# Optimization experiments

Measured on AMD Instinct MI355X. Metric: run time of the kernel, lower is better.

The kernel has to match this reference:

```python
import jax, jax.numpy as jnp
import numpy as np

QMAX = 127.0  # torch.iinfo(torch.int8).max


def setup_inputs() -> dict:
    key = jax.random.key(0)
    k1, k2 = jax.random.split(key)
    input_act = jax.random.normal(k1, (4, 2048, 4096), dtype=jnp.float32)
    # nn.Linear weight: [out_features, in_features], fp weights pre-quantization
    weight = jax.random.normal(k2, (4096, 4096), dtype=jnp.float32) * 0.02
    return {"input_act": input_act, "weight": weight}


def reference(input_act, weight):
    # --- weight_quant (per-channel over in_features) ---
    w_scale = jnp.max(jnp.abs(weight), axis=-1, keepdims=True) / QMAX      # [O, 1]
    w_q = jnp.round(weight / w_scale).astype(jnp.int8)                      # int8 weight

    # --- activation quant (per-token over last dim) ---
    a_scale = jnp.max(jnp.abs(input_act), axis=-1, keepdims=True) / QMAX    # [B, S, 1]
    x_q = jnp.round(input_act / a_scale).astype(jnp.int8)                   # int8 acts

    # --- int8 GEMM with int32 accumulation (torch._int_mm semantics) ---
    # [B, S, K] @ [K, O] -> [B, S, O]
    acc = jnp.matmul(x_q.astype(jnp.int32), w_q.T.astype(jnp.int32))        # exact int32

    # --- dequant: scale = input_act_scale * weight_scale.T, then cast to fp16 ---
    scale = a_scale * w_scale.T[None, :, :]                                 # [B, S, O]
    out = (acc.astype(jnp.float32) * scale).astype(jnp.float16)
    return out
```

## Files before the change

### kernel.cpp

```cpp
#include <hip/hip_runtime.h>
#include <hip/hip_fp16.h>
#include <cstdint>

typedef int v4i __attribute__((ext_vector_type(4)));

#define AS1C(p) ((const __attribute__((address_space(1))) void*)(p))
#define AS3(p)  ((__attribute__((address_space(3))) void*)(p))

__global__ __launch_bounds__(256) void quant_rows(const float* __restrict__ X,
                                                  int8_t* __restrict__ Q,
                                                  float* __restrict__ scales,
                                                  int K) {
    const int row = blockIdx.x;
    const float4* xv = (const float4*)(X + (size_t)row * K);

    float4 v[4];
#pragma unroll
    for (int j = 0; j < 4; ++j) v[j] = xv[threadIdx.x + (j << 8)];

    float m = 0.0f;
#pragma unroll
    for (int j = 0; j < 4; ++j) {
        m = fmaxf(m, fmaxf(fmaxf(fabsf(v[j].x), fabsf(v[j].y)),
                           fmaxf(fabsf(v[j].z), fabsf(v[j].w))));
    }
    for (int off = 32; off > 0; off >>= 1)
        m = fmaxf(m, __shfl_xor(m, off, 64));

    __shared__ float wmax[4];
    __shared__ float s_sc;
    const int lane = threadIdx.x & 63;
    const int wv = threadIdx.x >> 6;
    if (lane == 0) wmax[wv] = m;
    __syncthreads();
    if (threadIdx.x == 0) {
        float mm = fmaxf(fmaxf(wmax[0], wmax[1]), fmaxf(wmax[2], wmax[3]));
        float sc = mm / 127.0f;
        scales[row] = sc;
        s_sc = sc;
    }
    __syncthreads();
    const float sc = s_sc;

    char4* qv = (char4*)(Q + (size_t)row * K);
#pragma unroll
    for (int j = 0; j < 4; ++j) {
        char4 q;
        q.x = (signed char)(int)rintf(v[j].x / sc);
        q.y = (signed char)(int)rintf(v[j].y / sc);
        q.z = (signed char)(int)rintf(v[j].z / sc);
        q.w = (signed char)(int)rintf(v[j].w / sc);
        qv[threadIdx.x + (j << 8)] = q;
    }
}

__global__ __launch_bounds__(512, 2) void gemm_i8(const int8_t* __restrict__ Aq,
                                                  const int8_t* __restrict__ Bq,
                                                  const float* __restrict__ a_scale,
                                                  const float* __restrict__ w_scale,
                                                  float* __restrict__ out) {
    extern __shared__ __align__(16) int8_t smem[];

    const int K = 4096;
    const int bid = blockIdx.x;
    const int wg  = (bid & 7) * 64 + (bid >> 3);
    const int n0 = (wg & 15) * 256;
    const int m0 = (wg >> 4) * 256;

    const int tid  = threadIdx.x;
    const int lane = tid & 63;
    const int wid  = tid >> 6;
    const int wm   = wid >> 2;
    const int wn   = wid & 3;

    const int rsel  = lane & 15;
    const int kswz  = ((lane >> 4) << 4) ^ (((rsel >> 1) & 3) << 4);
    const int abase = (wm * 128 + rsel) * 64 + kswz;
    const int bbase = 16384 + (wn * 64 + rsel) * 64 + kswz;

    const int strow = tid >> 2;
    const int stswz = ((strow >> 1) & 3) << 4;
    const int stcol = ((tid & 3) << 4) ^ stswz;
    const int8_t* gA = Aq + (size_t)(m0 + strow) * K + stcol;
    const int8_t* gB = Bq + (size_t)(n0 + strow) * K + stcol;
    const size_t rstep = (size_t)128 * K;
    const int ldsst = wid * 1024;

    v4i acc[8][4] = {};
    v4i aFa[8], aFb[8], bFa[4], bFb[4];

#define STAGE(buf, kt) do {                                                          \
    int8_t* _d = smem + (buf) * 32768;                                               \
    const int8_t* _a = gA + (size_t)(kt) * 64;                                       \
    const int8_t* _b = gB + (size_t)(kt) * 64;                                       \
    __builtin_amdgcn_global_load_lds(AS1C(_a),         AS3(_d + ldsst),         16, 0, 0); \
    __builtin_amdgcn_global_load_lds(AS1C(_a + rstep), AS3(_d + 8192  + ldsst), 16, 0, 0); \
    __builtin_amdgcn_global_load_lds(AS1C(_b),         AS3(_d + 16384 + ldsst), 16, 0, 0); \
    __builtin_amdgcn_global_load_lds(AS1C(_b + rstep), AS3(_d + 24576 + ldsst), 16, 0, 0); \
  } while (0)

#define GROUP(g, CA, CB, NA, NB, gsrc, goff)  do {                                   \
    NA[2*(g)]     = *(const v4i*)(bufN + abase + (2*(g))     * 1024);                \
    NA[2*(g) + 1] = *(const v4i*)(bufN + abase + (2*(g) + 1) * 1024);                \
    NB[(g)]       = *(const v4i*)(bufN + bbase + (g) * 1024);                        \
    __builtin_amdgcn_global_load_lds(AS1C(gsrc), AS3(pD + (goff) + ldsst), 16, 0, 0);\
    _Pragma("unroll")                                                                \
    for (int nt = 0; nt < 4; ++nt) {                                                 \
        acc[2*(g)][nt] = __builtin_amdgcn_mfma_i32_16x16x64_i8(                      \
            CA[2*(g)], CB[nt], acc[2*(g)][nt], 0, 0, 0);                             \
        acc[2*(g)+1][nt] = __builtin_amdgcn_mfma_i32_16x16x64_i8(                    \
            CA[2*(g)+1], CB[nt], acc[2*(g)+1][nt], 0, 0, 0);                         \
    }                                                                                \
  } while (0)

#define KSTEP(u, CA, CB, NA, NB, kt4) do {                                           \
    const int kt  = (kt4) + (u);                                                     \
    const int8_t* bufN = smem + (((u) + 1) & 3) * 32768;                             \
    int8_t* pD = smem + (((u) + 3) & 3) * 32768;                                     \
    const int ktp = (kt + 3 < 64) ? (kt + 3) : 63;                                   \
    const int8_t* _a = gA + (size_t)ktp * 64;                                        \
    const int8_t* _b = gB + (size_t)ktp * 64;                                        \
    asm volatile("s_waitcnt vmcnt(4)" ::: "memory");                                 \
    __builtin_amdgcn_s_barrier();                                                    \
    __builtin_amdgcn_s_setprio(1);                                                   \
    GROUP(0, CA, CB, NA, NB, _a,         0);                                         \
    __builtin_amdgcn_sched_barrier(0);                                               \
    GROUP(1, CA, CB, NA, NB, _a + rstep, 8192);                                      \
    __builtin_amdgcn_sched_barrier(0);                                               \
    GROUP(2, CA, CB, NA, NB, _b,         16384);                                     \
    __builtin_amdgcn_sched_barrier(0);                                               \
    GROUP(3, CA, CB, NA, NB, _b + rstep, 24576);                                     \
    __builtin_amdgcn_s_setprio(0);                                                   \
  } while (0)

    STAGE(0, 0); STAGE(1, 1); STAGE(2, 2);
    asm volatile("s_waitcnt vmcnt(8)" ::: "memory");
    __builtin_amdgcn_s_barrier();
#pragma unroll
    for (int mt = 0; mt < 8; ++mt) aFa[mt] = *(const v4i*)(smem + abase + mt * 1024);
#pragma unroll
    for (int nt = 0; nt < 4; ++nt) bFa[nt] = *(const v4i*)(smem + bbase + nt * 1024);

    for (int kt4 = 0; kt4 < 64; kt4 += 4) {
        KSTEP(0, aFa, bFa, aFb, bFb, kt4);
        KSTEP(1, aFb, bFb, aFa, bFa, kt4);
        KSTEP(2, aFa, bFa, aFb, bFb, kt4);
        KSTEP(3, aFb, bFb, aFa, bFa, kt4);
    }

    const int r0  = (lane >> 4) << 2;
    const int col = lane & 15;
#pragma unroll
    for (int mt = 0; mt < 8; ++mt) {
        const int tbase = m0 + wm * 128 + mt * 16 + r0;
        float as[4];
#pragma unroll
        for (int r = 0; r < 4; ++r) as[r] = a_scale[tbase + r];
#pragma unroll
        for (int nt = 0; nt < 4; ++nt) {
            const int o = n0 + wn * 64 + nt * 16 + col;
            const float wsc = w_scale[o];
#pragma unroll
            for (int r = 0; r < 4; ++r) {
                float v = (float)acc[mt][nt][r] * as[r] * wsc;
                out[(size_t)(tbase + r) * 4096 + o] = __half2float(__float2half_rn(v));
            }
        }
    }
#undef KSTEP
#undef GROUP
#undef STAGE
}

extern "C" void kernel_launch(void* const* d_in, const int* in_sizes, int n_in,
                              void* d_out, int out_size, void* d_ws, size_t ws_size,
                              hipStream_t stream) {
    const float* input_act = (const float*)d_in[0];
    const float* weight    = (const float*)d_in[1];
    float* out = (float*)d_out;

    const int K = 4096, O = 4096, T = 8192;

    int8_t* x_q = (int8_t*)d_ws;
    int8_t* w_q = x_q + (size_t)T * K;
    float* a_scale = (float*)(w_q + (size_t)O * K);
    float* w_scale = a_scale + T;

    static bool attr_done = false;
    if (!attr_done) {
        hipFuncSetAttribute(reinterpret_cast<const void*>(gemm_i8),
                            hipFuncAttributeMaxDynamicSharedMemorySize, 131072);
        attr_done = true;
    }

    quant_rows<<<T, 256, 0, stream>>>(input_act, x_q, a_scale, K);
    quant_rows<<<O, 256, 0, stream>>>(weight, w_q, w_scale, K);

    dim3 grid(512);
    gemm_i8<<<grid, 512, 131072, stream>>>(x_q, w_q, a_scale, w_scale, out);
}
```

Before: 180.8 us.

## Fuse quant kernels and stagger MFMA/LDS-read phases across wave halves

Merges the activation and weight quantization launches into one kernel with a combined grid, removing one launch and the tail gap between them. In the GEMM main loop, the first four waves issue their LDS reads before the MFMAs in each group, while the other four waves issue MFMAs first and then reads. The setprio raise now wraps only the MFMA blocks. The intent is a ping-pong schedule in which one half of the waves keeps the matrix units busy while the other half loads fragments, at the cost of duplicated loop code and a changed register schedule.

```diff
diff --git a/kernel.cpp b/kernel.cpp
--- a/kernel.cpp
+++ b/kernel.cpp
@@ -7,12 +7,23 @@
 #define AS1C(p) ((const __attribute__((address_space(1))) void*)(p))
 #define AS3(p)  ((__attribute__((address_space(3))) void*)(p))
 
-__global__ __launch_bounds__(256) void quant_rows(const float* __restrict__ X,
-                                                  int8_t* __restrict__ Q,
-                                                  float* __restrict__ scales,
-                                                  int K) {
+__global__ __launch_bounds__(256) void quant_fused(const float* __restrict__ X,
+                                                   const float* __restrict__ W,
+                                                   int8_t* __restrict__ Xq,
+                                                   int8_t* __restrict__ Wq,
+                                                   float* __restrict__ a_scale,
+                                                   float* __restrict__ w_scale) {
     const int row = blockIdx.x;
-    const float4* xv = (const float4*)(X + (size_t)row * K);
+    const float* src;
+    int8_t* dst;
+    float* scp;
+    if (row < 8192) {
+        src = X + (size_t)row * 4096;  dst = Xq + (size_t)row * 4096;  scp = a_scale + row;
+    } else {
+        const int r = row - 8192;
+        src = W + (size_t)r * 4096;    dst = Wq + (size_t)r * 4096;    scp = w_scale + r;
+    }
+    const float4* xv = (const float4*)src;
 
     float4 v[4];
 #pragma unroll
@@ -36,13 +47,13 @@
     if (threadIdx.x == 0) {
         float mm = fmaxf(fmaxf(wmax[0], wmax[1]), fmaxf(wmax[2], wmax[3]));
         float sc = mm / 127.0f;
-        scales[row] = sc;
+        *scp = sc;
         s_sc = sc;
     }
     __syncthreads();
     const float sc = s_sc;
 
-    char4* qv = (char4*)(Q + (size_t)row * K);
+    char4* qv = (char4*)dst;
 #pragma unroll
     for (int j = 0; j < 4; ++j) {
         char4 q;
@@ -99,11 +110,15 @@
     __builtin_amdgcn_global_load_lds(AS1C(_b + rstep), AS3(_d + 24576 + ldsst), 16, 0, 0); \
   } while (0)
 
-#define GROUP(g, CA, CB, NA, NB, gsrc, goff)  do {                                   \
+#define READS(g, NA, NB, gsrc, goff) do {                                            \
     NA[2*(g)]     = *(const v4i*)(bufN + abase + (2*(g))     * 1024);                \
     NA[2*(g) + 1] = *(const v4i*)(bufN + abase + (2*(g) + 1) * 1024);                \
     NB[(g)]       = *(const v4i*)(bufN + bbase + (g) * 1024);                        \
     __builtin_amdgcn_global_load_lds(AS1C(gsrc), AS3(pD + (goff) + ldsst), 16, 0, 0);\
+  } while (0)
+
+#define MFMAS(g, CA, CB) do {                                                        \
+    __builtin_amdgcn_s_setprio(1);                                                   \
     _Pragma("unroll")                                                                \
     for (int nt = 0; nt < 4; ++nt) {                                                 \
         acc[2*(g)][nt] = __builtin_amdgcn_mfma_i32_16x16x64_i8(                      \
@@ -111,9 +126,24 @@
         acc[2*(g)+1][nt] = __builtin_amdgcn_mfma_i32_16x16x64_i8(                    \
             CA[2*(g)+1], CB[nt], acc[2*(g)+1][nt], 0, 0, 0);                         \
     }                                                                                \
-  } while (0)
-
-#define KSTEP(u, CA, CB, NA, NB, kt4) do {                                           \
+    __builtin_amdgcn_s_setprio(0);                                                   \
+  } while (0)
+
+#define GROUP_RW(g, CA, CB, NA, NB, gsrc, goff)  do {                                \
+    READS(g, NA, NB, gsrc, goff);                                                    \
+    __builtin_amdgcn_sched_barrier(0);                                               \
+    MFMAS(g, CA, CB);                                                                \
+    __builtin_amdgcn_sched_barrier(0);                                               \
+  } while (0)
+
+#define GROUP_WR(g, CA, CB, NA, NB, gsrc, goff)  do {                                \
+    MFMAS(g, CA, CB);                                                                \
+    __builtin_amdgcn_sched_barrier(0);                                               \
+    READS(g, NA, NB, gsrc, goff);                                                    \
+    __builtin_amdgcn_sched_barrier(0);                                               \
+  } while (0)
+
+#define KSTEP(G, u, CA, CB, NA, NB, kt4) do {                                        \
     const int kt  = (kt4) + (u);                                                     \
     const int8_t* bufN = smem + (((u) + 1) & 3) * 32768;                             \
     int8_t* pD = smem + (((u) + 3) & 3) * 32768;                                     \
@@ -122,15 +152,11 @@
     const int8_t* _b = gB + (size_t)ktp * 64;                                        \
     asm volatile("s_waitcnt vmcnt(4)" ::: "memory");                                 \
     __builtin_amdgcn_s_barrier();                                                    \
-    __builtin_amdgcn_s_setprio(1);                                                   \
-    GROUP(0, CA, CB, NA, NB, _a,         0);                                         \
-    __builtin_amdgcn_sched_barrier(0);                                               \
-    GROUP(1, CA, CB, NA, NB, _a + rstep, 8192);                                      \
-    __builtin_amdgcn_sched_barrier(0);                                               \
-    GROUP(2, CA, CB, NA, NB, _b,         16384);                                     \
-    __builtin_amdgcn_sched_barrier(0);                                               \
-    GROUP(3, CA, CB, NA, NB, _b + rstep, 24576);                                     \
-    __builtin_amdgcn_s_setprio(0);                                                   \
+    __builtin_amdgcn_sched_barrier(0);                                               \
+    G(0, CA, CB, NA, NB, _a,         0);                                             \
+    G(1, CA, CB, NA, NB, _a + rstep, 8192);                                          \
+    G(2, CA, CB, NA, NB, _b,         16384);                                         \
+    G(3, CA, CB, NA, NB, _b + rstep, 24576);                                         \
   } while (0)
 
     STAGE(0, 0); STAGE(1, 1); STAGE(2, 2);
@@ -141,11 +167,20 @@
 #pragma unroll
     for (int nt = 0; nt < 4; ++nt) bFa[nt] = *(const v4i*)(smem + bbase + nt * 1024);
 
-    for (int kt4 = 0; kt4 < 64; kt4 += 4) {
-        KSTEP(0, aFa, bFa, aFb, bFb, kt4);
-        KSTEP(1, aFb, bFb, aFa, bFa, kt4);
-        KSTEP(2, aFa, bFa, aFb, bFb, kt4);
-        KSTEP(3, aFb, bFb, aFa, bFa, kt4);
+    if (wid < 4) {
+        for (int kt4 = 0; kt4 < 64; kt4 += 4) {
+            KSTEP(GROUP_RW, 0, aFa, bFa, aFb, bFb, kt4);
+            KSTEP(GROUP_RW, 1, aFb, bFb, aFa, bFa, kt4);
+            KSTEP(GROUP_RW, 2, aFa, bFa, aFb, bFb, kt4);
+            KSTEP(GROUP_RW, 3, aFb, bFb, aFa, bFa, kt4);
+        }
+    } else {
+        for (int kt4 = 0; kt4 < 64; kt4 += 4) {
+            KSTEP(GROUP_WR, 0, aFa, bFa, aFb, bFb, kt4);
+            KSTEP(GROUP_WR, 1, aFb, bFb, aFa, bFa, kt4);
+            KSTEP(GROUP_WR, 2, aFa, bFa, aFb, bFb, kt4);
+            KSTEP(GROUP_WR, 3, aFb, bFb, aFa, bFa, kt4);
+        }
     }
 
     const int r0  = (lane >> 4) << 2;
@@ -168,7 +203,10 @@
         }
     }
 #undef KSTEP
-#undef GROUP
+#undef GROUP_RW
+#undef GROUP_WR
+#undef MFMAS
+#undef READS
 #undef STAGE
 }
 
@@ -193,8 +231,8 @@
         attr_done = true;
     }
 
-    quant_rows<<<T, 256, 0, stream>>>(input_act, x_q, a_scale, K);
-    quant_rows<<<O, 256, 0, stream>>>(weight, w_q, w_scale, K);
+    quant_fused<<<T + O, 256, 0, stream>>>(input_act, weight, x_q, w_q,
+                                           a_scale, w_scale);
 
     dim3 grid(512);
     gemm_i8<<<grid, 512, 131072, stream>>>(x_q, w_q, a_scale, w_scale, out);
```

New measurement: 177.1 us (median of 2 runs). 1.02x faster.
